# Kernel optimization log

Measured on AMD Instinct MI355X. Metric: run time of the kernel, lower is better.

## Reference

```python
import jax, jax.numpy as jnp
import numpy as np

B, C_IN, N, HC = 32, 128, 8192, 64
HEAD_NAMES = ['hm', 'reg', 'height', 'dim', 'rot', 'iou']
HEAD_OUT = [3, 2, 1, 3, 2, 1]
EPS = 1e-5
INIT_BIAS = -2.19


def setup_inputs() -> dict:
    key = jax.random.key(0)
    ks = jax.random.split(key, 16)
    d = {}
    d['ct_feat'] = jax.random.normal(ks[0], (B, C_IN, N), jnp.float32)
    # shared conv (1x1) + BN1d params
    d['sh_w'] = jax.random.normal(ks[1], (HC, C_IN), jnp.float32) * 0.05
    d['sh_b'] = jnp.zeros((HC,), jnp.float32)
    d['sh_g'] = jnp.ones((HC,), jnp.float32)
    d['sh_beta'] = jnp.zeros((HC,), jnp.float32)
    d['sh_mean'] = jax.random.normal(ks[2], (HC,), jnp.float32) * 0.1
    d['sh_var'] = jax.random.uniform(ks[3], (HC,), jnp.float32) + 0.5
    # first conv layer of each SepHead branch (stacked over 6 heads)
    d['head_w1'] = jax.random.normal(ks[4], (6, HC, HC), jnp.float32) * 0.05
    d['head_b1'] = jnp.zeros((6, HC), jnp.float32)
    d['head_g1'] = jnp.ones((6, HC), jnp.float32)
    d['head_beta1'] = jnp.zeros((6, HC), jnp.float32)
    d['head_mean1'] = jax.random.normal(ks[5], (6, HC), jnp.float32) * 0.1
    d['head_var1'] = jax.random.uniform(ks[6], (6, HC), jnp.float32) + 0.5
    # final conv of each branch (distinct out channels)
    for i, (name, c_out) in enumerate(zip(HEAD_NAMES, HEAD_OUT)):
        d[name + '_w'] = jax.random.normal(ks[7 + i], (c_out, HC), jnp.float32) * 0.05
        if name == 'hm':  # hm final bias is filled with init_bias
            d[name + '_b'] = jnp.full((c_out,), INIT_BIAS, jnp.float32)
        else:
            d[name + '_b'] = jnp.zeros((c_out,), jnp.float32)
    return d


def _bn(x, g, b, m, v):
    # x: [B, C, N]; params: [C]
    return (x - m[:, None]) * jax.lax.rsqrt(v[:, None] + EPS) * g[:, None] + b[:, None]


def reference(ct_feat, sh_w, sh_b, sh_g, sh_beta, sh_mean, sh_var,
              head_w1, head_b1, head_g1, head_beta1, head_mean1, head_var1,
              hm_w, hm_b, reg_w, reg_b, height_w, height_b,
              dim_w, dim_b, rot_w, rot_b, iou_w, iou_b):
    # shared_conv: Conv1d(k=1) + BN1d + ReLU
    y = jnp.einsum('oc,bcn->bon', sh_w, ct_feat) + sh_b[:, None]
    y = jax.nn.relu(_bn(y, sh_g, sh_beta, sh_mean, sh_var))  # [B, HC, N]

    # first layer of all 6 head branches, batched over head axis h
    z = jnp.einsum('hoc,bcn->hbon', head_w1, y) + head_b1[:, None, :, None]
    z = (z - head_mean1[:, None, :, None]) * jax.lax.rsqrt(head_var1[:, None, :, None] + EPS)
    z = z * head_g1[:, None, :, None] + head_beta1[:, None, :, None]
    z = jax.nn.relu(z)  # [6, B, HC, N]

    finals = [(hm_w, hm_b), (reg_w, reg_b), (height_w, height_b),
              (dim_w, dim_b), (rot_w, rot_b), (iou_w, iou_b)]
    outs = [jnp.einsum('oc,bcn->bon', w, z[i]) + b[:, None]
            for i, (w, b) in enumerate(finals)]
    # concat in head order [hm(3), reg(2), height(1), dim(3), rot(2), iou(1)] -> [B, 12, N]
    return jnp.concatenate(outs, axis=1)
```

## Files before the change

### kernel.cpp

```cpp
#include <hip/hip_runtime.h>
#include <hip/hip_bf16.h>
#include <cstdint>

typedef __attribute__((ext_vector_type(8))) short bf16x8;
typedef __attribute__((ext_vector_type(4))) float f32x4;

#define NCOL 8192

#define WS_AW 0
#define WS_A1 8192
#define WS_AF 32768
#define WS_U16_TOTAL 38912
#define WS_OFSH 19456
#define WS_OFH  19520
#define WS_BIAS 19904
#define PREP_TOTAL (WS_U16_TOTAL + 464)

union FragU { uint32_t u[4]; bf16x8 v; uint4 q; };

__device__ __forceinline__ uint16_t f2bf(float f) {
  uint32_t x = __builtin_bit_cast(uint32_t, f);
  x += 0x7fffu + ((x >> 16) & 1u);
  return (uint16_t)(x >> 16);
}
__device__ __forceinline__ uint32_t rne_bits(float f) {
  uint32_t x = __builtin_bit_cast(uint32_t, f);
  return x + 0x7fffu + ((x >> 16) & 1u);
}
__device__ __forceinline__ uint32_t pack_bf16(float lo, float hi) {
  return __builtin_amdgcn_perm(rne_bits(hi), rne_bits(lo), 0x07060302u);
}

__global__ __launch_bounds__(256) void ch_prep(
    const float* __restrict__ shw, const float* __restrict__ shb,
    const float* __restrict__ shg, const float* __restrict__ shbeta,
    const float* __restrict__ shmean, const float* __restrict__ shvar,
    const float* __restrict__ w1, const float* __restrict__ b1,
    const float* __restrict__ g1, const float* __restrict__ beta1,
    const float* __restrict__ mean1, const float* __restrict__ var1,
    const float* __restrict__ hm_w, const float* __restrict__ hm_b,
    const float* __restrict__ reg_w, const float* __restrict__ reg_b,
    const float* __restrict__ height_w, const float* __restrict__ height_b,
    const float* __restrict__ dim_w, const float* __restrict__ dim_b,
    const float* __restrict__ rot_w, const float* __restrict__ rot_b,
    const float* __restrict__ iou_w, const float* __restrict__ iou_b,
    uint16_t* __restrict__ wsq)
{
  const int e = blockIdx.x * 256 + threadIdx.x;
  if (e >= PREP_TOTAL) return;
  const int rowbase[6] = {0, 3, 5, 6, 9, 11};
  const int couts[6]   = {3, 2, 1, 3, 2, 1};
  const float* wfp[6]  = {hm_w, reg_w, height_w, dim_w, rot_w, iou_w};

  if (e < WS_A1) {
    const int i = e & 7, q = (e >> 3) & 3, kc = (e >> 5) & 3, m = e >> 7;
    const int k = kc * 32 + q * 8 + i;
    const float sc = shg[m] * rsqrtf(shvar[m] + 1e-5f);
    wsq[e] = f2bf(shw[m * 128 + k] * sc);
  } else if (e < WS_AF) {
    const int e2 = e - WS_A1;
    const int i = e2 & 7, q = (e2 >> 3) & 3, kc = (e2 >> 5) & 1,
              m = (e2 >> 6) & 63, h = e2 >> 12;
    const int k = kc * 32 + q * 8 + i, row = h * 64 + m;
    const float sc = g1[row] * rsqrtf(var1[row] + 1e-5f);
    wsq[e] = f2bf(w1[row * 64 + k] * sc);
  } else if (e < WS_U16_TOTAL) {
    const int e2 = e - WS_AF;
    const int i = e2 & 7, q = (e2 >> 3) & 3, kc = (e2 >> 5) & 1,
              m = (e2 >> 6) & 15, h = e2 >> 10;
    const int k = kc * 32 + q * 8 + i, rr = m - rowbase[h];
    const float v = (rr >= 0 && rr < couts[h]) ? wfp[h][rr * 64 + k] : 0.f;
    wsq[e] = f2bf(v);
  } else {
    const int t2 = e - WS_U16_TOTAL;
    float* wff = (float*)wsq;
    float v = 0.f;
    if (t2 < 64) {
      const float sc = shg[t2] * rsqrtf(shvar[t2] + 1e-5f);
      v = (shb[t2] - shmean[t2]) * sc + shbeta[t2];
    } else if (t2 < 448) {
      const int i = t2 - 64;
      const float sc = g1[i] * rsqrtf(var1[i] + 1e-5f);
      v = (b1[i] - mean1[i]) * sc + beta1[i];
    } else {
      const int i = t2 - 448;
      if (i < 3)       v = hm_b[i];
      else if (i < 5)  v = reg_b[i - 3];
      else if (i < 6)  v = height_b[i - 5];
      else if (i < 9)  v = dim_b[i - 6];
      else if (i < 11) v = rot_b[i - 9];
      else if (i < 12) v = iou_b[i - 11];
    }
    wff[WS_OFSH + t2] = v;
  }
}

__global__ __launch_bounds__(256, 4) void ch_main(
    const float* __restrict__ ct,
    const uint16_t* __restrict__ wsq,
    const float* __restrict__ wsf,
    float* __restrict__ outp)
{
  __shared__ __align__(16) uint32_t sm_y[4608];
  __shared__ __align__(16) uint32_t sm_z[4608];

  const int t    = threadIdx.x;
  const int wv   = t >> 6;
  const int lane = t & 63;
  const int l15  = lane & 15;
  const int qd   = lane >> 4;
  const int bid  = blockIdx.x;
  const int b    = bid >> 6;
  const int col0 = (bid & 63) * 128;
  const int nb   = wv * 32;

  const float* ctb = ct + (size_t)b * 128 * NCOL;
  const int voff0 = qd * 8 * NCOL + col0 + nb + l15;

  f32x4 accY[4][2];
  #pragma unroll
  for (int mt = 0; mt < 4; ++mt)
    #pragma unroll
    for (int j = 0; j < 2; ++j)
      accY[mt][j] = (f32x4){0.f, 0.f, 0.f, 0.f};

  #pragma unroll
  for (int kc = 0; kc < 4; ++kc) {
    bf16x8 a[4];
    #pragma unroll
    for (int mt = 0; mt < 4; ++mt) {
      FragU fa;
      fa.q = *(const uint4*)(wsq + WS_AW + ((mt * 16 + l15) * 4 + kc) * 32 + qd * 8);
      a[mt] = fa.v;
    }
    #pragma unroll
    for (int j = 0; j < 2; ++j) {
      FragU f;
      #pragma unroll
      for (int i2 = 0; i2 < 4; ++i2) {
        const size_t off = (size_t)((kc * 32 + 2 * i2) * NCOL) + voff0 + j * 16;
        f.u[i2] = pack_bf16(ctb[off], ctb[off + NCOL]);
      }
      #pragma unroll
      for (int mt = 0; mt < 4; ++mt)
        accY[mt][j] = __builtin_amdgcn_mfma_f32_16x16x32_bf16(a[mt], f.v, accY[mt][j], 0, 0, 0);
    }
  }

  #pragma unroll
  for (int mt = 0; mt < 4; ++mt) {
    const f32x4 of = *(const f32x4*)(wsf + WS_OFSH + mt * 16 + qd * 4);
    #pragma unroll
    for (int j = 0; j < 2; ++j) {
      const f32x4 v = accY[mt][j];
      const float y0 = fmaxf(v[0] + of[0], 0.f);
      const float y1 = fmaxf(v[1] + of[1], 0.f);
      const float y2 = fmaxf(v[2] + of[2], 0.f);
      const float y3 = fmaxf(v[3] + of[3], 0.f);
      uint2 val;
      val.x = pack_bf16(y0, y1);
      val.y = pack_bf16(y2, y3);
      *(uint2*)&sm_y[(nb + j * 16 + l15) * 36 + mt * 8 + qd * 2] = val;
    }
  }

  f32x4 accO[2];
  accO[0] = (f32x4){0.f, 0.f, 0.f, 0.f};
  accO[1] = (f32x4){0.f, 0.f, 0.f, 0.f};

  #pragma unroll
  for (int h = 0; h < 6; ++h) {
    f32x4 accZ[4][2];
    #pragma unroll
    for (int mt = 0; mt < 4; ++mt)
      #pragma unroll
      for (int j = 0; j < 2; ++j)
        accZ[mt][j] = (f32x4){0.f, 0.f, 0.f, 0.f};

    #pragma unroll
    for (int kc = 0; kc < 2; ++kc) {
      bf16x8 a[4];
      #pragma unroll
      for (int mt = 0; mt < 4; ++mt) {
        FragU fa;
        fa.q = *(const uint4*)(wsq + WS_A1 + ((h * 64 + mt * 16 + l15) * 2 + kc) * 32 + qd * 8);
        a[mt] = fa.v;
      }
      #pragma unroll
      for (int j = 0; j < 2; ++j) {
        FragU f;
        f.q = *(const uint4*)&sm_y[(nb + j * 16 + l15) * 36 + kc * 16 + qd * 4];
        #pragma unroll
        for (int mt = 0; mt < 4; ++mt)
          accZ[mt][j] = __builtin_amdgcn_mfma_f32_16x16x32_bf16(a[mt], f.v, accZ[mt][j], 0, 0, 0);
      }
    }

    #pragma unroll
    for (int mt = 0; mt < 4; ++mt) {
      const f32x4 of = *(const f32x4*)(wsf + WS_OFH + h * 64 + mt * 16 + qd * 4);
      #pragma unroll
      for (int j = 0; j < 2; ++j) {
        const f32x4 v = accZ[mt][j];
        const float z0 = fmaxf(v[0] + of[0], 0.f);
        const float z1 = fmaxf(v[1] + of[1], 0.f);
        const float z2 = fmaxf(v[2] + of[2], 0.f);
        const float z3 = fmaxf(v[3] + of[3], 0.f);
        uint2 val;
        val.x = pack_bf16(z0, z1);
        val.y = pack_bf16(z2, z3);
        *(uint2*)&sm_z[(nb + j * 16 + l15) * 36 + mt * 8 + qd * 2] = val;
      }
    }

    #pragma unroll
    for (int kc = 0; kc < 2; ++kc) {
      FragU fa;
      fa.q = *(const uint4*)(wsq + WS_AF + ((h * 16 + l15) * 2 + kc) * 32 + qd * 8);
      #pragma unroll
      for (int j = 0; j < 2; ++j) {
        FragU f;
        f.q = *(const uint4*)&sm_z[(nb + j * 16 + l15) * 36 + kc * 16 + qd * 4];
        accO[j] = __builtin_amdgcn_mfma_f32_16x16x32_bf16(fa.v, f.v, accO[j], 0, 0, 0);
      }
    }
  }

  if (qd < 3) {
    const f32x4 bs = *(const f32x4*)(wsf + WS_BIAS + qd * 4);
    #pragma unroll
    for (int j = 0; j < 2; ++j) {
      const int col = col0 + nb + j * 16 + l15;
      #pragma unroll
      for (int r = 0; r < 4; ++r)
        outp[((size_t)(b * 12 + qd * 4 + r)) * NCOL + col] = accO[j][r] + bs[r];
    }
  }
}

extern "C" void kernel_launch(void* const* d_in, const int* in_sizes, int n_in,
                              void* d_out, int out_size, void* d_ws, size_t ws_size,
                              hipStream_t stream) {
  (void)out_size; (void)ws_size;
  static const int sortedPos[25] = {
      0, 24, 19, 21, 20, 22, 23, 8, 3, 5, 4, 6, 7,
      12, 11, 16, 15, 10, 9, 2, 1, 18, 17, 14, 13};
  const bool sorted_order =
      (n_in == 25) && (in_sizes[1] == 3) && (in_sizes[2] == 192) &&
      (in_sizes[8] == 24576) && (in_sizes[24] == 8192);
  const float* p[25];
  for (int r = 0; r < 25; ++r)
    p[r] = (const float*)d_in[sorted_order ? sortedPos[r] : r];

  uint16_t* wsq = (uint16_t*)d_ws;

  hipLaunchKernelGGL(ch_prep, dim3((PREP_TOTAL + 255) / 256), dim3(256), 0, stream,
      p[1], p[2], p[3], p[4], p[5], p[6],
      p[7], p[8], p[9], p[10], p[11], p[12],
      p[13], p[14], p[15], p[16], p[17], p[18],
      p[19], p[20], p[21], p[22], p[23], p[24],
      wsq);

  hipLaunchKernelGGL(ch_main, dim3(2048), dim3(256), 0, stream,
      p[0], (const uint16_t*)wsq, (const float*)wsq, (float*)d_out);
}
```

Measured before the change: 294.7 us.

## Preload input tile into registers, double-buffer head weights, vectorize prep

Issues all 64 global loads of the input feature tile up front into registers before any MFMA work, so memory latency overlaps instead of being interleaved with compute. Head first-layer weight fragments are double-buffered, with the next head prefetched during the current head's MFMAs, and final-layer weights are loaded before the epilogue. The launch bounds drop from 4 to 3 waves-per-EU to make room for the larger register footprint, and the prep kernel now processes 8 elements per thread with float4 loads and a smaller grid. The risk is lower occupancy and register pressure, which could reduce latency hiding elsewhere.

```diff
diff --git a/kernel.cpp b/kernel.cpp
--- a/kernel.cpp
+++ b/kernel.cpp
@@ -6,6 +6,7 @@
 typedef __attribute__((ext_vector_type(4))) float f32x4;
 
 #define NCOL 8192
+#define YST 36
 
 #define WS_AW 0
 #define WS_A1 8192
@@ -14,15 +15,9 @@
 #define WS_OFSH 19456
 #define WS_OFH  19520
 #define WS_BIAS 19904
-#define PREP_TOTAL (WS_U16_TOTAL + 464)
 
 union FragU { uint32_t u[4]; bf16x8 v; uint4 q; };
 
-__device__ __forceinline__ uint16_t f2bf(float f) {
-  uint32_t x = __builtin_bit_cast(uint32_t, f);
-  x += 0x7fffu + ((x >> 16) & 1u);
-  return (uint16_t)(x >> 16);
-}
 __device__ __forceinline__ uint32_t rne_bits(float f) {
   uint32_t x = __builtin_bit_cast(uint32_t, f);
   return x + 0x7fffu + ((x >> 16) & 1u);
@@ -46,33 +41,52 @@
     const float* __restrict__ iou_w, const float* __restrict__ iou_b,
     uint16_t* __restrict__ wsq)
 {
-  const int e = blockIdx.x * 256 + threadIdx.x;
-  if (e >= PREP_TOTAL) return;
+  const int tid = blockIdx.x * 256 + threadIdx.x;
   const int rowbase[6] = {0, 3, 5, 6, 9, 11};
   const int couts[6]   = {3, 2, 1, 3, 2, 1};
-  const float* wfp[6]  = {hm_w, reg_w, height_w, dim_w, rot_w, iou_w};
-
-  if (e < WS_A1) {
-    const int i = e & 7, q = (e >> 3) & 3, kc = (e >> 5) & 3, m = e >> 7;
-    const int k = kc * 32 + q * 8 + i;
-    const float sc = shg[m] * rsqrtf(shvar[m] + 1e-5f);
-    wsq[e] = f2bf(shw[m * 128 + k] * sc);
-  } else if (e < WS_AF) {
-    const int e2 = e - WS_A1;
-    const int i = e2 & 7, q = (e2 >> 3) & 3, kc = (e2 >> 5) & 1,
-              m = (e2 >> 6) & 63, h = e2 >> 12;
-    const int k = kc * 32 + q * 8 + i, row = h * 64 + m;
-    const float sc = g1[row] * rsqrtf(var1[row] + 1e-5f);
-    wsq[e] = f2bf(w1[row * 64 + k] * sc);
-  } else if (e < WS_U16_TOTAL) {
-    const int e2 = e - WS_AF;
-    const int i = e2 & 7, q = (e2 >> 3) & 3, kc = (e2 >> 5) & 1,
-              m = (e2 >> 6) & 15, h = e2 >> 10;
-    const int k = kc * 32 + q * 8 + i, rr = m - rowbase[h];
-    const float v = (rr >= 0 && rr < couts[h]) ? wfp[h][rr * 64 + k] : 0.f;
-    wsq[e] = f2bf(v);
-  } else {
-    const int t2 = e - WS_U16_TOTAL;
+
+  if (tid < WS_U16_TOTAL / 8) {
+    const int e = tid * 8;
+    const float* src = nullptr;
+    float sc = 1.f;
+    if (e < WS_A1) {
+      const int q = (e >> 3) & 3, kc = (e >> 5) & 3, m = e >> 7;
+      sc = shg[m] * rsqrtf(shvar[m] + 1e-5f);
+      src = shw + m * 128 + kc * 32 + q * 8;
+    } else if (e < WS_AF) {
+      const int e2 = e - WS_A1;
+      const int q = (e2 >> 3) & 3, kc = (e2 >> 5) & 1, m = (e2 >> 6) & 63, h = e2 >> 12;
+      const int row = h * 64 + m;
+      sc = g1[row] * rsqrtf(var1[row] + 1e-5f);
+      src = w1 + row * 64 + kc * 32 + q * 8;
+    } else {
+      const int e2 = e - WS_AF;
+      const int q = (e2 >> 3) & 3, kc = (e2 >> 5) & 1, m = (e2 >> 6) & 15, h = e2 >> 10;
+      const int rr = m - rowbase[h];
+      if (rr >= 0 && rr < couts[h]) {
+        const float* wp;
+        switch (h) {
+          case 0: wp = hm_w; break;   case 1: wp = reg_w; break;
+          case 2: wp = height_w; break; case 3: wp = dim_w; break;
+          case 4: wp = rot_w; break;  default: wp = iou_w; break;
+        }
+        src = wp + rr * 64 + kc * 32 + q * 8;
+      }
+    }
+    uint4 out;
+    if (src) {
+      const float4 a = *(const float4*)src;
+      const float4 b = *(const float4*)(src + 4);
+      out.x = pack_bf16(a.x * sc, a.y * sc);
+      out.y = pack_bf16(a.z * sc, a.w * sc);
+      out.z = pack_bf16(b.x * sc, b.y * sc);
+      out.w = pack_bf16(b.z * sc, b.w * sc);
+    } else {
+      out = make_uint4(0, 0, 0, 0);
+    }
+    *(uint4*)(wsq + e) = out;
+  } else if (tid < WS_U16_TOTAL / 8 + 464) {
+    const int t2 = tid - WS_U16_TOTAL / 8;
     float* wff = (float*)wsq;
     float v = 0.f;
     if (t2 < 64) {
@@ -95,14 +109,14 @@
   }
 }
 
-__global__ __launch_bounds__(256, 4) void ch_main(
+__global__ __launch_bounds__(256, 3) void ch_main(
     const float* __restrict__ ct,
     const uint16_t* __restrict__ wsq,
     const float* __restrict__ wsf,
     float* __restrict__ outp)
 {
-  __shared__ __align__(16) uint32_t sm_y[4608];
-  __shared__ __align__(16) uint32_t sm_z[4608];
+  __shared__ __align__(16) uint32_t sm_y[128 * YST];
+  __shared__ __align__(16) uint32_t sm_z[128 * YST];
 
   const int t    = threadIdx.x;
   const int wv   = t >> 6;
@@ -114,8 +128,19 @@
   const int col0 = (bid & 63) * 128;
   const int nb   = wv * 32;
 
-  const float* ctb = ct + (size_t)b * 128 * NCOL;
-  const int voff0 = qd * 8 * NCOL + col0 + nb + l15;
+  const float* xl = ct + (size_t)b * 128 * NCOL + qd * 8 * NCOL + col0 + nb + l15;
+
+  float r[4][2][8];
+  #pragma unroll
+  for (int kc = 0; kc < 4; ++kc)
+    #pragma unroll
+    for (int j = 0; j < 2; ++j)
+      #pragma unroll
+      for (int i2 = 0; i2 < 4; ++i2) {
+        const size_t off = (size_t)((kc * 32 + 2 * i2) * NCOL) + j * 16;
+        r[kc][j][2 * i2]     = xl[off];
+        r[kc][j][2 * i2 + 1] = xl[off + NCOL];
+      }
 
   f32x4 accY[4][2];
   #pragma unroll
@@ -126,24 +151,19 @@
 
   #pragma unroll
   for (int kc = 0; kc < 4; ++kc) {
-    bf16x8 a[4];
-    #pragma unroll
-    for (int mt = 0; mt < 4; ++mt) {
-      FragU fa;
-      fa.q = *(const uint4*)(wsq + WS_AW + ((mt * 16 + l15) * 4 + kc) * 32 + qd * 8);
-      a[mt] = fa.v;
-    }
+    FragU aw[4];
+    #pragma unroll
+    for (int mt = 0; mt < 4; ++mt)
+      aw[mt].q = *(const uint4*)(wsq + WS_AW + ((mt * 16 + l15) * 4 + kc) * 32 + qd * 8);
     #pragma unroll
     for (int j = 0; j < 2; ++j) {
       FragU f;
       #pragma unroll
-      for (int i2 = 0; i2 < 4; ++i2) {
-        const size_t off = (size_t)((kc * 32 + 2 * i2) * NCOL) + voff0 + j * 16;
-        f.u[i2] = pack_bf16(ctb[off], ctb[off + NCOL]);
-      }
+      for (int i2 = 0; i2 < 4; ++i2)
+        f.u[i2] = pack_bf16(r[kc][j][2 * i2], r[kc][j][2 * i2 + 1]);
       #pragma unroll
       for (int mt = 0; mt < 4; ++mt)
-        accY[mt][j] = __builtin_amdgcn_mfma_f32_16x16x32_bf16(a[mt], f.v, accY[mt][j], 0, 0, 0);
+        accY[mt][j] = __builtin_amdgcn_mfma_f32_16x16x32_bf16(aw[mt].v, f.v, accY[mt][j], 0, 0, 0);
     }
   }
 
@@ -153,16 +173,22 @@
     #pragma unroll
     for (int j = 0; j < 2; ++j) {
       const f32x4 v = accY[mt][j];
-      const float y0 = fmaxf(v[0] + of[0], 0.f);
-      const float y1 = fmaxf(v[1] + of[1], 0.f);
-      const float y2 = fmaxf(v[2] + of[2], 0.f);
-      const float y3 = fmaxf(v[3] + of[3], 0.f);
       uint2 val;
-      val.x = pack_bf16(y0, y1);
-      val.y = pack_bf16(y2, y3);
-      *(uint2*)&sm_y[(nb + j * 16 + l15) * 36 + mt * 8 + qd * 2] = val;
-    }
-  }
+      val.x = pack_bf16(fmaxf(v[0] + of[0], 0.f), fmaxf(v[1] + of[1], 0.f));
+      val.y = pack_bf16(fmaxf(v[2] + of[2], 0.f), fmaxf(v[3] + of[3], 0.f));
+      *(uint2*)&sm_y[(nb + j * 16 + l15) * YST + mt * 8 + qd * 2] = val;
+    }
+  }
+
+  FragU a1[2][4][2];
+  auto load_a1 = [&](int h, FragU (&d)[4][2]) {
+    #pragma unroll
+    for (int mt = 0; mt < 4; ++mt)
+      #pragma unroll
+      for (int kc = 0; kc < 2; ++kc)
+        d[mt][kc].q = *(const uint4*)(wsq + WS_A1 + ((h * 64 + mt * 16 + l15) * 2 + kc) * 32 + qd * 8);
+  };
+  load_a1(0, a1[0]);
 
   f32x4 accO[2];
   accO[0] = (f32x4){0.f, 0.f, 0.f, 0.f};
@@ -170,6 +196,9 @@
 
   #pragma unroll
   for (int h = 0; h < 6; ++h) {
+    const int cur = h & 1;
+    if (h < 5) load_a1(h + 1, a1[cur ^ 1]);
+
     f32x4 accZ[4][2];
     #pragma unroll
     for (int mt = 0; mt < 4; ++mt)
@@ -179,22 +208,20 @@
 
     #pragma unroll
     for (int kc = 0; kc < 2; ++kc) {
-      bf16x8 a[4];
-      #pragma unroll
-      for (int mt = 0; mt < 4; ++mt) {
-        FragU fa;
-        fa.q = *(const uint4*)(wsq + WS_A1 + ((h * 64 + mt * 16 + l15) * 2 + kc) * 32 + qd * 8);
-        a[mt] = fa.v;
-      }
       #pragma unroll
       for (int j = 0; j < 2; ++j) {
         FragU f;
-        f.q = *(const uint4*)&sm_y[(nb + j * 16 + l15) * 36 + kc * 16 + qd * 4];
+        f.q = *(const uint4*)&sm_y[(nb + j * 16 + l15) * YST + kc * 16 + qd * 4];
         #pragma unroll
         for (int mt = 0; mt < 4; ++mt)
-          accZ[mt][j] = __builtin_amdgcn_mfma_f32_16x16x32_bf16(a[mt], f.v, accZ[mt][j], 0, 0, 0);
-      }
-    }
+          accZ[mt][j] = __builtin_amdgcn_mfma_f32_16x16x32_bf16(a1[cur][mt][kc].v, f.v, accZ[mt][j], 0, 0, 0);
+      }
+    }
+
+    FragU af[2];
+    #pragma unroll
+    for (int kc = 0; kc < 2; ++kc)
+      af[kc].q = *(const uint4*)(wsq + WS_AF + ((h * 16 + l15) * 2 + kc) * 32 + qd * 8);
 
     #pragma unroll
     for (int mt = 0; mt < 4; ++mt) {
@@ -202,26 +229,20 @@
       #pragma unroll
       for (int j = 0; j < 2; ++j) {
         const f32x4 v = accZ[mt][j];
-        const float z0 = fmaxf(v[0] + of[0], 0.f);
-        const float z1 = fmaxf(v[1] + of[1], 0.f);
-        const float z2 = fmaxf(v[2] + of[2], 0.f);
-        const float z3 = fmaxf(v[3] + of[3], 0.f);
         uint2 val;
-        val.x = pack_bf16(z0, z1);
-        val.y = pack_bf16(z2, z3);
-        *(uint2*)&sm_z[(nb + j * 16 + l15) * 36 + mt * 8 + qd * 2] = val;
+        val.x = pack_bf16(fmaxf(v[0] + of[0], 0.f), fmaxf(v[1] + of[1], 0.f));
+        val.y = pack_bf16(fmaxf(v[2] + of[2], 0.f), fmaxf(v[3] + of[3], 0.f));
+        *(uint2*)&sm_z[(nb + j * 16 + l15) * YST + mt * 8 + qd * 2] = val;
       }
     }
 
     #pragma unroll
     for (int kc = 0; kc < 2; ++kc) {
-      FragU fa;
-      fa.q = *(const uint4*)(wsq + WS_AF + ((h * 16 + l15) * 2 + kc) * 32 + qd * 8);
       #pragma unroll
       for (int j = 0; j < 2; ++j) {
         FragU f;
-        f.q = *(const uint4*)&sm_z[(nb + j * 16 + l15) * 36 + kc * 16 + qd * 4];
-        accO[j] = __builtin_amdgcn_mfma_f32_16x16x32_bf16(fa.v, f.v, accO[j], 0, 0, 0);
+        f.q = *(const uint4*)&sm_z[(nb + j * 16 + l15) * YST + kc * 16 + qd * 4];
+        accO[j] = __builtin_amdgcn_mfma_f32_16x16x32_bf16(af[kc].v, f.v, accO[j], 0, 0, 0);
       }
     }
   }
@@ -232,8 +253,8 @@
     for (int j = 0; j < 2; ++j) {
       const int col = col0 + nb + j * 16 + l15;
       #pragma unroll
-      for (int r = 0; r < 4; ++r)
-        outp[((size_t)(b * 12 + qd * 4 + r)) * NCOL + col] = accO[j][r] + bs[r];
+      for (int r2 = 0; r2 < 4; ++r2)
+        outp[((size_t)(b * 12 + qd * 4 + r2)) * NCOL + col] = accO[j][r2] + bs[r2];
     }
   }
 }
@@ -254,7 +275,7 @@
 
   uint16_t* wsq = (uint16_t*)d_ws;
 
-  hipLaunchKernelGGL(ch_prep, dim3((PREP_TOTAL + 255) / 256), dim3(256), 0, stream,
+  hipLaunchKernelGGL(ch_prep, dim3(21), dim3(256), 0, stream,
       p[1], p[2], p[3], p[4], p[5], p[6],
       p[7], p[8], p[9], p[10], p[11], p[12],
       p[13], p[14], p[15], p[16], p[17], p[18],
```

New measurement: 298.0 us. About the same (+1.1%).
